# Performance work log

Measured on AMD Instinct MI355X. Metric: run time of the kernel, lower is better.

## Reference

```python
import jax, jax.numpy as jnp
import numpy as np

BATCH = 1048576
D_IN = 4        # d_in=3 spatial dims + 1 time dim
HID = 64
N_HID_STACK = 4  # hidden residual blocks after the first hidden layer
D_OUT = 3
BN_EPS = 1e-5


def _bn(x, gamma, beta):
    # BatchNorm1d in training mode: biased batch statistics over the batch axis
    mu = jnp.mean(x, axis=0)
    var = jnp.var(x, axis=0)
    return gamma * (x - mu) * jax.lax.rsqrt(var + BN_EPS) + beta


def setup_inputs() -> dict:
    key = jax.random.key(0)
    ks = jax.random.split(key, 8)
    s_in = 1.0 / np.sqrt(D_IN)
    s_h = 1.0 / np.sqrt(HID)
    return {
        "x": jax.random.normal(ks[0], (BATCH, D_IN), dtype=jnp.float32),
        "bn0_gamma": jnp.ones((D_IN,), jnp.float32),
        "bn0_beta": jnp.zeros((D_IN,), jnp.float32),
        "W0": jax.random.normal(ks[1], (D_IN, HID), jnp.float32) * s_in,
        "b0": jnp.zeros((HID,), jnp.float32),
        "gamma0": jnp.ones((HID,), jnp.float32),
        "beta0": jnp.zeros((HID,), jnp.float32),
        "W_hid": jax.random.normal(ks[2], (N_HID_STACK, HID, HID), jnp.float32) * s_h,
        "b_hid": jnp.zeros((N_HID_STACK, HID), jnp.float32),
        "gamma_hid": jnp.ones((N_HID_STACK, HID), jnp.float32),
        "beta_hid": jnp.zeros((N_HID_STACK, HID), jnp.float32),
        "Wout": jax.random.normal(ks[3], (HID, D_OUT), jnp.float32) * s_h,
        "bout": jnp.zeros((D_OUT,), jnp.float32),
    }


def reference(x, bn0_gamma, bn0_beta, W0, b0, gamma0, beta0,
              W_hid, b_hid, gamma_hid, beta_hid, Wout, bout):
    # Net.forward (u-network, single patch, batch_normalization=True, tanh):
    #   x = bn0(x)
    #   y = bn(act(Linear0(x)))                 (first hidden layer, no skip)
    #   y = bn_i(act(Linear_i(y))) + y          (residual hidden layers)
    #   y = Linear_out(y)
    h = _bn(x, bn0_gamma, bn0_beta)
    y = _bn(jnp.tanh(h @ W0 + b0), gamma0, beta0)

    def step(y, layer):
        W, b, g, be = layer
        return _bn(jnp.tanh(y @ W + b), g, be) + y, None

    y, _ = jax.lax.scan(step, y, (W_hid, b_hid, gamma_hid, beta_hid))
    return y @ Wout + bout
```

## Files before the change

### kernel.cpp

```cpp
#include <hip/hip_runtime.h>
#include <stdint.h>


#define NROWS 1048576
#define EPS 1e-5f
#define INV_B 9.5367431640625e-07f
#define LOG2E2 2.885390081777927f

typedef __attribute__((ext_vector_type(8))) short bfrag;
typedef __attribute__((ext_vector_type(4))) float facc;
typedef __attribute__((ext_vector_type(4))) float f4v;

__device__ __forceinline__ float bf2f(short s) {
  union { unsigned u; float f; } v;
  v.u = ((unsigned)(unsigned short)s) << 16;
  return v.f;
}
__device__ __forceinline__ short f2bf(float f) {
  union { float f; unsigned u; } v;
  v.f = f;
  unsigned r = v.u + 0x7FFFu + ((v.u >> 16) & 1u);
  return (short)(r >> 16);
}
__device__ __forceinline__ float tanh_fast(float x) {
  float e = __builtin_amdgcn_exp2f(x * LOG2E2);
  return 1.f - 2.f * __builtin_amdgcn_rcpf(e + 1.f);
}

template <int W>
__global__ __launch_bounds__(256) void k_reduce(const float* __restrict__ P,
                                                float* __restrict__ S,
                                                int rows_per_blk) {
  __shared__ float red[256];
  const int tid = threadIdx.x;
  const int col = tid % W;
  const int grp = tid / W;
  const int G = 256 / W;
  size_t r0 = (size_t)blockIdx.x * rows_per_blk;
  float s = 0.f;
  for (int r = grp; r < rows_per_blk; r += G) s += P[(r0 + r) * W + col];
  red[tid] = s;
  __syncthreads();
  if (tid < W) {
    float t = 0.f;
#pragma unroll 4
    for (int g = 0; g < G; ++g) t += red[g * W + tid];
    atomicAdd(&S[tid], t);
  }
}


__global__ __launch_bounds__(256) void k_stats_x(const float* __restrict__ x,
                                                 float* __restrict__ P) {
  __shared__ float red[4][8];
  const int tid = threadIdx.x;
  const int wave = tid >> 6;
  size_t base = (size_t)blockIdx.x * 1024 + tid;
  float s[4] = {0.f, 0.f, 0.f, 0.f}, q[4] = {0.f, 0.f, 0.f, 0.f};
#pragma unroll
  for (int it = 0; it < 4; ++it) {
    f4v v = *(const f4v*)(x + (base + (size_t)it * 256) * 4);
#pragma unroll
    for (int k = 0; k < 4; ++k) { s[k] += v[k]; q[k] = fmaf(v[k], v[k], q[k]); }
  }
#pragma unroll
  for (int off = 32; off > 0; off >>= 1) {
#pragma unroll
    for (int k = 0; k < 4; ++k) {
      s[k] += __shfl_xor(s[k], off);
      q[k] += __shfl_xor(q[k], off);
    }
  }
  if ((tid & 63) == 0) {
#pragma unroll
    for (int k = 0; k < 4; ++k) { red[wave][k] = s[k]; red[wave][4 + k] = q[k]; }
  }
  __syncthreads();
  if (tid < 8)
    P[blockIdx.x * 8 + tid] =
        red[0][tid] + red[1][tid] + red[2][tid] + red[3][tid];
}

__global__ __launch_bounds__(256) void k_stats_z1(
    const float* __restrict__ x, const float* __restrict__ bn0g,
    const float* __restrict__ bn0b, const float* __restrict__ W0,
    const float* __restrict__ b0, const float* __restrict__ sx,
    float* __restrict__ P) {
  __shared__ float red[2][4][64];
  const int tid = threadIdx.x;
  const int lane = tid & 63;
  const int wave = tid >> 6;
  int gw = blockIdx.x * 4 + wave;
  float sc[4], sh[4];
#pragma unroll
  for (int k = 0; k < 4; ++k) {
    float mean = sx[k] * INV_B;
    float var = fmaf(-mean, mean, sx[4 + k] * INV_B);
    float rs = rsqrtf(var + EPS);
    sc[k] = bn0g[k] * rs;
    sh[k] = fmaf(-sc[k], mean, bn0b[k]);
  }
  float w[4];
#pragma unroll
  for (int k = 0; k < 4; ++k) w[k] = W0[k * 64 + lane];
  float bj = b0[lane];
  float s = 0.f, q = 0.f;
  size_t r0 = (size_t)gw * 256;
  for (int r = 0; r < 256; ++r) {
    f4v xv = *(const f4v*)(x + (r0 + r) * 4);
    float acc = bj;
#pragma unroll
    for (int k = 0; k < 4; ++k)
      acc = fmaf(fmaf(xv[k], sc[k], sh[k]), w[k], acc);
    float z = tanh_fast(acc);
    s += z;
    q = fmaf(z, z, q);
  }
  red[0][wave][lane] = s;
  red[1][wave][lane] = q;
  __syncthreads();
  if (tid < 128) {
    int which = tid >> 6, c = tid & 63;
    P[blockIdx.x * 128 + tid] = red[which][0][c] + red[which][1][c] +
                                red[which][2][c] + red[which][3][c];
  }
}

__global__ __launch_bounds__(256) void k_prep(const float* __restrict__ Wh,
                                              short* __restrict__ WT) {
  int idx = blockIdx.x * 256 + threadIdx.x;
  int l = idx >> 12, rem = idx & 4095, k = rem >> 6, c = rem & 63;
  WT[l * 4096 + c * 64 + k] = f2bf(Wh[l * 4096 + k * 64 + c]);
}


__global__ __launch_bounds__(256) void k_first(
    const float* __restrict__ x, const float* __restrict__ bn0g,
    const float* __restrict__ bn0b, const float* __restrict__ W0,
    const float* __restrict__ b0, const float* __restrict__ gamma0,
    const float* __restrict__ beta0, const float* __restrict__ sx,
    const float* __restrict__ s1, const short* __restrict__ WTb,
    const float* __restrict__ bb, float* __restrict__ P,
    short* __restrict__ Y) {
  __shared__ __align__(16) float lds_x[128 * 4];
  __shared__ float lds_W0[256];
  __shared__ float lds_b0[64], lds_A1[64], lds_B1[64], lds_bb[64];
  __shared__ float lds_s0[4], lds_sh0[4];
  __shared__ __align__(16) short lds_y[128 * 72];
  __shared__ float lds_st[128];

  const int tid = threadIdx.x;
  const int lane = tid & 63;
  const int wave = tid >> 6;
  const int l15 = lane & 15;
  const int q = lane >> 4;
  const size_t r0 = (size_t)blockIdx.x * 128;

  if (tid < 128) {
    *(f4v*)(lds_x + tid * 4) = *(const f4v*)(x + (r0 + tid) * 4);
    lds_st[tid] = 0.f;
  }
  lds_W0[tid] = W0[tid];
  if (tid < 64) {
    lds_b0[tid] = b0[tid];
    float mean = s1[tid] * INV_B;
    float var = fmaf(-mean, mean, s1[64 + tid] * INV_B);
    float rs = rsqrtf(var + EPS);
    float A = gamma0[tid] * rs;
    lds_A1[tid] = A;
    lds_B1[tid] = fmaf(-A, mean, beta0[tid]);
    lds_bb[tid] = bb[tid];
  }
  if (tid < 4) {
    float mean = sx[tid] * INV_B;
    float var = fmaf(-mean, mean, sx[4 + tid] * INV_B);
    float rs = rsqrtf(var + EPS);
    float sc = bn0g[tid] * rs;
    lds_s0[tid] = sc;
    lds_sh0[tid] = fmaf(-sc, mean, bn0b[tid]);
  }
  __syncthreads();

  const int wr = wave * 32;
  float sc0[4], sh0[4];
#pragma unroll
  for (int k = 0; k < 4; ++k) { sc0[k] = lds_s0[k]; sh0[k] = lds_sh0[k]; }
  for (int e = 0; e < 32; ++e) {
    int row = wr + e;
    float acc = lds_b0[lane];
#pragma unroll
    for (int k = 0; k < 4; ++k)
      acc = fmaf(fmaf(lds_x[row * 4 + k], sc0[k], sh0[k]),
                 lds_W0[k * 64 + lane], acc);
    float z = tanh_fast(acc);
    lds_y[row * 72 + lane] = f2bf(fmaf(lds_A1[lane], z, lds_B1[lane]));
  }

  bfrag a2[2][2], bw[4][2];
#pragma unroll
  for (int mt = 0; mt < 2; ++mt)
#pragma unroll
    for (int kt = 0; kt < 2; ++kt) {
      a2[mt][kt] =
          *(const bfrag*)&lds_y[(wr + mt * 16 + l15) * 72 + kt * 32 + q * 8];
      *(bfrag*)(Y + (r0 + wr + mt * 16 + l15) * 64 + kt * 32 + q * 8) =
          a2[mt][kt];
    }
#pragma unroll
  for (int nt = 0; nt < 4; ++nt)
#pragma unroll
    for (int kt = 0; kt < 2; ++kt)
      bw[nt][kt] = *(const bfrag*)(WTb + (nt * 16 + l15) * 64 + kt * 32 + q * 8);
  facc acc2[2][4];
#pragma unroll
  for (int mt = 0; mt < 2; ++mt)
#pragma unroll
    for (int nt = 0; nt < 4; ++nt) {
      float bias = lds_bb[nt * 16 + l15];
      acc2[mt][nt][0] = bias; acc2[mt][nt][1] = bias;
      acc2[mt][nt][2] = bias; acc2[mt][nt][3] = bias;
    }
#pragma unroll
  for (int mt = 0; mt < 2; ++mt)
#pragma unroll
    for (int nt = 0; nt < 4; ++nt)
#pragma unroll
      for (int kt = 0; kt < 2; ++kt)
        acc2[mt][nt] = __builtin_amdgcn_mfma_f32_16x16x32_bf16(
            a2[mt][kt], bw[nt][kt], acc2[mt][nt], 0, 0, 0);
#pragma unroll
  for (int nt = 0; nt < 4; ++nt) {
    float s = 0.f, ss = 0.f;
#pragma unroll
    for (int mt = 0; mt < 2; ++mt)
#pragma unroll
      for (int i = 0; i < 4; ++i) {
        float z = tanh_fast(acc2[mt][nt][i]);
        s += z;
        ss = fmaf(z, z, ss);
      }
    s += __shfl_xor(s, 16); s += __shfl_xor(s, 32);
    ss += __shfl_xor(ss, 16); ss += __shfl_xor(ss, 32);
    if (q == 0) {
      atomicAdd(&lds_st[nt * 16 + l15], s);
      atomicAdd(&lds_st[64 + nt * 16 + l15], ss);
    }
  }
  __syncthreads();
  if (tid < 128) P[(size_t)blockIdx.x * 128 + tid] = lds_st[tid];
}

__global__ __launch_bounds__(256) void k_mid(
    short* __restrict__ Y, const short* __restrict__ WTa,
    const float* __restrict__ ba, const float* __restrict__ ga,
    const float* __restrict__ bea, const float* __restrict__ sa,
    const short* __restrict__ WTb, const float* __restrict__ bb,
    float* __restrict__ P) {
  __shared__ __align__(16) short lds_y[128 * 72];
  __shared__ float lds_A[64], lds_Bc[64], lds_ba[64], lds_bb[64];
  __shared__ float lds_st[128];

  const int tid = threadIdx.x;
  const int lane = tid & 63;
  const int wave = tid >> 6;
  const int l15 = lane & 15;
  const int q = lane >> 4;
  const size_t r0 = (size_t)blockIdx.x * 128;

#pragma unroll
  for (int it = 0; it < 4; ++it) {
    int chunk = it * 256 + tid;
    int row = chunk >> 3;
    int c8 = (chunk & 7) * 8;
    *(bfrag*)&lds_y[row * 72 + c8] = *(const bfrag*)(Y + (r0 + row) * 64 + c8);
  }
  if (tid < 128) lds_st[tid] = 0.f;
  if (tid < 64) {
    float mean = sa[tid] * INV_B;
    float var = fmaf(-mean, mean, sa[64 + tid] * INV_B);
    float rs = rsqrtf(var + EPS);
    float A = ga[tid] * rs;
    lds_A[tid] = A;
    lds_Bc[tid] = fmaf(-A, mean, bea[tid]);
    lds_ba[tid] = ba[tid];
    lds_bb[tid] = bb[tid];
  }
  __syncthreads();

  const int wr = wave * 32;
  bfrag a1[2][2], bw[4][2];
#pragma unroll
  for (int mt = 0; mt < 2; ++mt)
#pragma unroll
    for (int kt = 0; kt < 2; ++kt)
      a1[mt][kt] =
          *(const bfrag*)&lds_y[(wr + mt * 16 + l15) * 72 + kt * 32 + q * 8];
#pragma unroll
  for (int nt = 0; nt < 4; ++nt)
#pragma unroll
    for (int kt = 0; kt < 2; ++kt)
      bw[nt][kt] = *(const bfrag*)(WTa + (nt * 16 + l15) * 64 + kt * 32 + q * 8);
  facc acc[2][4];
#pragma unroll
  for (int mt = 0; mt < 2; ++mt)
#pragma unroll
    for (int nt = 0; nt < 4; ++nt) {
      float bias = lds_ba[nt * 16 + l15];
      acc[mt][nt][0] = bias; acc[mt][nt][1] = bias;
      acc[mt][nt][2] = bias; acc[mt][nt][3] = bias;
    }
#pragma unroll
  for (int mt = 0; mt < 2; ++mt)
#pragma unroll
    for (int nt = 0; nt < 4; ++nt)
#pragma unroll
      for (int kt = 0; kt < 2; ++kt)
        acc[mt][nt] = __builtin_amdgcn_mfma_f32_16x16x32_bf16(
            a1[mt][kt], bw[nt][kt], acc[mt][nt], 0, 0, 0);

#pragma unroll
  for (int mt = 0; mt < 2; ++mt)
#pragma unroll
    for (int nt = 0; nt < 4; ++nt) {
      int c = nt * 16 + l15;
      float A = lds_A[c], Bc = lds_Bc[c];
#pragma unroll
      for (int i = 0; i < 4; ++i) {
        int rl = wr + mt * 16 + q * 4 + i;
        float z = tanh_fast(acc[mt][nt][i]);
        float yo = bf2f(lds_y[rl * 72 + c]);
        lds_y[rl * 72 + c] = f2bf(fmaf(A, z, Bc) + yo);
      }
    }

  bfrag a2[2][2];
#pragma unroll
  for (int mt = 0; mt < 2; ++mt)
#pragma unroll
    for (int kt = 0; kt < 2; ++kt) {
      a2[mt][kt] =
          *(const bfrag*)&lds_y[(wr + mt * 16 + l15) * 72 + kt * 32 + q * 8];
      *(bfrag*)(Y + (r0 + wr + mt * 16 + l15) * 64 + kt * 32 + q * 8) =
          a2[mt][kt];
    }
#pragma unroll
  for (int nt = 0; nt < 4; ++nt)
#pragma unroll
    for (int kt = 0; kt < 2; ++kt)
      bw[nt][kt] = *(const bfrag*)(WTb + (nt * 16 + l15) * 64 + kt * 32 + q * 8);
  facc acc2[2][4];
#pragma unroll
  for (int mt = 0; mt < 2; ++mt)
#pragma unroll
    for (int nt = 0; nt < 4; ++nt) {
      float bias = lds_bb[nt * 16 + l15];
      acc2[mt][nt][0] = bias; acc2[mt][nt][1] = bias;
      acc2[mt][nt][2] = bias; acc2[mt][nt][3] = bias;
    }
#pragma unroll
  for (int mt = 0; mt < 2; ++mt)
#pragma unroll
    for (int nt = 0; nt < 4; ++nt)
#pragma unroll
      for (int kt = 0; kt < 2; ++kt)
        acc2[mt][nt] = __builtin_amdgcn_mfma_f32_16x16x32_bf16(
            a2[mt][kt], bw[nt][kt], acc2[mt][nt], 0, 0, 0);
#pragma unroll
  for (int nt = 0; nt < 4; ++nt) {
    float s = 0.f, ss = 0.f;
#pragma unroll
    for (int mt = 0; mt < 2; ++mt)
#pragma unroll
      for (int i = 0; i < 4; ++i) {
        float z = tanh_fast(acc2[mt][nt][i]);
        s += z;
        ss = fmaf(z, z, ss);
      }
    s += __shfl_xor(s, 16); s += __shfl_xor(s, 32);
    ss += __shfl_xor(ss, 16); ss += __shfl_xor(ss, 32);
    if (q == 0) {
      atomicAdd(&lds_st[nt * 16 + l15], s);
      atomicAdd(&lds_st[64 + nt * 16 + l15], ss);
    }
  }
  __syncthreads();
  if (tid < 128) P[(size_t)blockIdx.x * 128 + tid] = lds_st[tid];
}

__global__ __launch_bounds__(256) void k_last(
    const short* __restrict__ Y, const short* __restrict__ WTa,
    const float* __restrict__ ba, const float* __restrict__ ga,
    const float* __restrict__ bea, const float* __restrict__ sa,
    const float* __restrict__ Wout, const float* __restrict__ bout,
    float* __restrict__ out) {
  __shared__ __align__(16) short lds_y[128 * 72];
  __shared__ float lds_A[64], lds_Bc[64], lds_ba[64];
  __shared__ float lds_wo[192];
  __shared__ float lds_bo[3];

  const int tid = threadIdx.x;
  const int lane = tid & 63;
  const int wave = tid >> 6;
  const int l15 = lane & 15;
  const int q = lane >> 4;
  const size_t r0 = (size_t)blockIdx.x * 128;

#pragma unroll
  for (int it = 0; it < 4; ++it) {
    int chunk = it * 256 + tid;
    int row = chunk >> 3;
    int c8 = (chunk & 7) * 8;
    *(bfrag*)&lds_y[row * 72 + c8] = *(const bfrag*)(Y + (r0 + row) * 64 + c8);
  }
  if (tid < 64) {
    float mean = sa[tid] * INV_B;
    float var = fmaf(-mean, mean, sa[64 + tid] * INV_B);
    float rs = rsqrtf(var + EPS);
    float A = ga[tid] * rs;
    lds_A[tid] = A;
    lds_Bc[tid] = fmaf(-A, mean, bea[tid]);
    lds_ba[tid] = ba[tid];
  }
  if (tid < 192) lds_wo[tid] = Wout[tid];
  if (tid < 3) lds_bo[tid] = bout[tid];
  __syncthreads();

  const int wr = wave * 32;
  bfrag a1[2][2], bw[4][2];
#pragma unroll
  for (int mt = 0; mt < 2; ++mt)
#pragma unroll
    for (int kt = 0; kt < 2; ++kt)
      a1[mt][kt] =
          *(const bfrag*)&lds_y[(wr + mt * 16 + l15) * 72 + kt * 32 + q * 8];
#pragma unroll
  for (int nt = 0; nt < 4; ++nt)
#pragma unroll
    for (int kt = 0; kt < 2; ++kt)
      bw[nt][kt] = *(const bfrag*)(WTa + (nt * 16 + l15) * 64 + kt * 32 + q * 8);
  facc acc[2][4];
#pragma unroll
  for (int mt = 0; mt < 2; ++mt)
#pragma unroll
    for (int nt = 0; nt < 4; ++nt) {
      float bias = lds_ba[nt * 16 + l15];
      acc[mt][nt][0] = bias; acc[mt][nt][1] = bias;
      acc[mt][nt][2] = bias; acc[mt][nt][3] = bias;
    }
#pragma unroll
  for (int mt = 0; mt < 2; ++mt)
#pragma unroll
    for (int nt = 0; nt < 4; ++nt)
#pragma unroll
      for (int kt = 0; kt < 2; ++kt)
        acc[mt][nt] = __builtin_amdgcn_mfma_f32_16x16x32_bf16(
            a1[mt][kt], bw[nt][kt], acc[mt][nt], 0, 0, 0);
#pragma unroll
  for (int mt = 0; mt < 2; ++mt)
#pragma unroll
    for (int nt = 0; nt < 4; ++nt) {
      int c = nt * 16 + l15;
      float A = lds_A[c], Bc = lds_Bc[c];
#pragma unroll
      for (int i = 0; i < 4; ++i) {
        int rl = wr + mt * 16 + q * 4 + i;
        float z = tanh_fast(acc[mt][nt][i]);
        float yo = bf2f(lds_y[rl * 72 + c]);
        lds_y[rl * 72 + c] = f2bf(fmaf(A, z, Bc) + yo);
      }
    }
  __syncthreads();

  if (tid < 128) {
    float o0 = lds_bo[0], o1 = lds_bo[1], o2 = lds_bo[2];
#pragma unroll
    for (int jc = 0; jc < 8; ++jc) {
      bfrag v = *(const bfrag*)&lds_y[tid * 72 + jc * 8];
#pragma unroll
      for (int j = 0; j < 8; ++j) {
        float f = bf2f(v[j]);
        int jj = jc * 8 + j;
        o0 = fmaf(f, lds_wo[jj * 3 + 0], o0);
        o1 = fmaf(f, lds_wo[jj * 3 + 1], o1);
        o2 = fmaf(f, lds_wo[jj * 3 + 2], o2);
      }
    }
    size_t ro = (r0 + tid) * 3;
    out[ro] = o0;
    out[ro + 1] = o1;
    out[ro + 2] = o2;
  }
}

extern "C" void kernel_launch(void* const* d_in, const int* in_sizes, int n_in,
                              void* d_out, int out_size, void* d_ws,
                              size_t ws_size, hipStream_t stream) {
  (void)in_sizes; (void)n_in; (void)out_size; (void)ws_size;
  const float* x = (const float*)d_in[0];
  const float* bn0g = (const float*)d_in[1];
  const float* bn0b = (const float*)d_in[2];
  const float* W0 = (const float*)d_in[3];
  const float* b0 = (const float*)d_in[4];
  const float* gamma0 = (const float*)d_in[5];
  const float* beta0 = (const float*)d_in[6];
  const float* Wh = (const float*)d_in[7];
  const float* bh = (const float*)d_in[8];
  const float* gh = (const float*)d_in[9];
  const float* beh = (const float*)d_in[10];
  const float* Wout = (const float*)d_in[11];
  const float* bout = (const float*)d_in[12];
  float* out = (float*)d_out;

  char* ws = (char*)d_ws;
  short* Y = (short*)ws;
  const size_t YB = (size_t)NROWS * 64 * 2;
  float* stats = (float*)(ws + YB);
  float* Sx = stats;
  float* S1 = stats + 8;
  float* S2 = stats + 136;
  float* S3 = stats + 264;
  float* S4 = stats + 392;
  float* S5 = stats + 520;
  short* WT = (short*)(ws + YB + 4096);
  float* P = (float*)(ws + YB + 4096 + 32768);

  hipMemsetAsync(stats, 0, 648 * sizeof(float), stream);
  k_prep<<<64, 256, 0, stream>>>(Wh, WT);
  k_stats_x<<<1024, 256, 0, stream>>>(x, P);
  k_reduce<8><<<8, 256, 0, stream>>>(P, Sx, 128);
  k_stats_z1<<<1024, 256, 0, stream>>>(x, bn0g, bn0b, W0, b0, Sx, P);
  k_reduce<128><<<8, 256, 0, stream>>>(P, S1, 128);
  k_first<<<8192, 256, 0, stream>>>(x, bn0g, bn0b, W0, b0, gamma0, beta0, Sx,
                                    S1, WT, bh, P, Y);
  k_reduce<128><<<64, 256, 0, stream>>>(P, S2, 128);
  k_mid<<<8192, 256, 0, stream>>>(Y, WT, bh, gh, beh, S2, WT + 4096, bh + 64,
                                  P);
  k_reduce<128><<<64, 256, 0, stream>>>(P, S3, 128);
  k_mid<<<8192, 256, 0, stream>>>(Y, WT + 4096, bh + 64, gh + 64, beh + 64, S3,
                                  WT + 2 * 4096, bh + 128, P);
  k_reduce<128><<<64, 256, 0, stream>>>(P, S4, 128);
  k_mid<<<8192, 256, 0, stream>>>(Y, WT + 2 * 4096, bh + 128, gh + 128,
                                  beh + 128, S4, WT + 3 * 4096, bh + 192, P);
  k_reduce<128><<<64, 256, 0, stream>>>(P, S5, 128);
  k_last<<<8192, 256, 0, stream>>>(Y, WT + 3 * 4096, bh + 192, gh + 192,
                                   beh + 192, S5, Wout, bout, out);
}
```

Before: 568.6 us.

## Process four row tiles per block with register prefetch and hoisted weights

Each block of the first, middle and last kernels now handles four 128-row tiles in a loop. Per-column BN coefficients, biases and bf16 weight fragments are loaded into registers once per block instead of through LDS for every tile. The next tile's activations are prefetched into registers while the current tile is computed, and BN statistics accumulate across tiles, so the grid and the partial-sum reductions shrink by four. The output projection is spread over all lanes with a shuffle reduction. Risks are higher register pressure (launch bounds request 3 blocks per SM) and fewer blocks to hide memory latency.

```diff
diff --git a/kernel.cpp b/kernel.cpp
--- a/kernel.cpp
+++ b/kernel.cpp
@@ -6,6 +6,8 @@
 #define EPS 1e-5f
 #define INV_B 9.5367431640625e-07f
 #define LOG2E2 2.885390081777927f
+#define TILES 4
+#define BIGGRID 2048
 
 typedef __attribute__((ext_vector_type(8))) short bfrag;
 typedef __attribute__((ext_vector_type(4))) float facc;
@@ -134,7 +136,7 @@
 }
 
 
-__global__ __launch_bounds__(256) void k_first(
+__global__ __launch_bounds__(256, 3) void k_first(
     const float* __restrict__ x, const float* __restrict__ bn0g,
     const float* __restrict__ bn0b, const float* __restrict__ W0,
     const float* __restrict__ b0, const float* __restrict__ gamma0,
@@ -143,9 +145,6 @@
     const float* __restrict__ bb, float* __restrict__ P,
     short* __restrict__ Y) {
   __shared__ __align__(16) float lds_x[128 * 4];
-  __shared__ float lds_W0[256];
-  __shared__ float lds_b0[64], lds_A1[64], lds_B1[64], lds_bb[64];
-  __shared__ float lds_s0[4], lds_sh0[4];
   __shared__ __align__(16) short lds_y[128 * 72];
   __shared__ float lds_st[128];
 
@@ -154,91 +153,102 @@
   const int wave = tid >> 6;
   const int l15 = lane & 15;
   const int q = lane >> 4;
-  const size_t r0 = (size_t)blockIdx.x * 128;
-
-  if (tid < 128) {
-    *(f4v*)(lds_x + tid * 4) = *(const f4v*)(x + (r0 + tid) * 4);
-    lds_st[tid] = 0.f;
-  }
-  lds_W0[tid] = W0[tid];
-  if (tid < 64) {
-    lds_b0[tid] = b0[tid];
-    float mean = s1[tid] * INV_B;
-    float var = fmaf(-mean, mean, s1[64 + tid] * INV_B);
+  const int wr = wave * 32;
+
+  if (tid < 128) lds_st[tid] = 0.f;
+  float sc0[4], sh0[4];
+#pragma unroll
+  for (int k = 0; k < 4; ++k) {
+    float mean = sx[k] * INV_B;
+    float var = fmaf(-mean, mean, sx[4 + k] * INV_B);
     float rs = rsqrtf(var + EPS);
-    float A = gamma0[tid] * rs;
-    lds_A1[tid] = A;
-    lds_B1[tid] = fmaf(-A, mean, beta0[tid]);
-    lds_bb[tid] = bb[tid];
-  }
-  if (tid < 4) {
-    float mean = sx[tid] * INV_B;
-    float var = fmaf(-mean, mean, sx[4 + tid] * INV_B);
-    float rs = rsqrtf(var + EPS);
-    float sc = bn0g[tid] * rs;
-    lds_s0[tid] = sc;
-    lds_sh0[tid] = fmaf(-sc, mean, bn0b[tid]);
-  }
-  __syncthreads();
-
-  const int wr = wave * 32;
-  float sc0[4], sh0[4];
-#pragma unroll
-  for (int k = 0; k < 4; ++k) { sc0[k] = lds_s0[k]; sh0[k] = lds_sh0[k]; }
-  for (int e = 0; e < 32; ++e) {
-    int row = wr + e;
-    float acc = lds_b0[lane];
-#pragma unroll
-    for (int k = 0; k < 4; ++k)
-      acc = fmaf(fmaf(lds_x[row * 4 + k], sc0[k], sh0[k]),
-                 lds_W0[k * 64 + lane], acc);
-    float z = tanh_fast(acc);
-    lds_y[row * 72 + lane] = f2bf(fmaf(lds_A1[lane], z, lds_B1[lane]));
-  }
-
-  bfrag a2[2][2], bw[4][2];
-#pragma unroll
-  for (int mt = 0; mt < 2; ++mt)
-#pragma unroll
-    for (int kt = 0; kt < 2; ++kt) {
-      a2[mt][kt] =
-          *(const bfrag*)&lds_y[(wr + mt * 16 + l15) * 72 + kt * 32 + q * 8];
-      *(bfrag*)(Y + (r0 + wr + mt * 16 + l15) * 64 + kt * 32 + q * 8) =
-          a2[mt][kt];
-    }
-#pragma unroll
-  for (int nt = 0; nt < 4; ++nt)
+    sc0[k] = bn0g[k] * rs;
+    sh0[k] = fmaf(-sc0[k], mean, bn0b[k]);
+  }
+  float w0c[4];
+#pragma unroll
+  for (int k = 0; k < 4; ++k) w0c[k] = W0[k * 64 + lane];
+  float b0c = b0[lane];
+  float mean1 = s1[lane] * INV_B;
+  float var1 = fmaf(-mean1, mean1, s1[64 + lane] * INV_B);
+  float A1c = gamma0[lane] * rsqrtf(var1 + EPS);
+  float B1c = fmaf(-A1c, mean1, beta0[lane]);
+  float bbv[4];
+  bfrag bwb[4][2];
+#pragma unroll
+  for (int nt = 0; nt < 4; ++nt) {
+    bbv[nt] = bb[nt * 16 + l15];
 #pragma unroll
     for (int kt = 0; kt < 2; ++kt)
-      bw[nt][kt] = *(const bfrag*)(WTb + (nt * 16 + l15) * 64 + kt * 32 + q * 8);
-  facc acc2[2][4];
-#pragma unroll
-  for (int mt = 0; mt < 2; ++mt)
-#pragma unroll
-    for (int nt = 0; nt < 4; ++nt) {
-      float bias = lds_bb[nt * 16 + l15];
-      acc2[mt][nt][0] = bias; acc2[mt][nt][1] = bias;
-      acc2[mt][nt][2] = bias; acc2[mt][nt][3] = bias;
-    }
-#pragma unroll
-  for (int mt = 0; mt < 2; ++mt)
+      bwb[nt][kt] =
+          *(const bfrag*)(WTb + (nt * 16 + l15) * 64 + kt * 32 + q * 8);
+  }
+  __syncthreads();
+
+  float sAcc[4] = {0.f, 0.f, 0.f, 0.f}, qAcc[4] = {0.f, 0.f, 0.f, 0.f};
+  const size_t tbase = (size_t)blockIdx.x * TILES * 128;
+
+  f4v xp;
+  if (lane < 32) xp = *(const f4v*)(x + (tbase + wr + lane) * 4);
+
+#pragma unroll
+  for (int t = 0; t < TILES; ++t) {
+    const size_t r0 = tbase + (size_t)t * 128;
+    if (lane < 32) *(f4v*)&lds_x[(wr + lane) * 4] = xp;
+    if (t + 1 < TILES && lane < 32)
+      xp = *(const f4v*)(x + (r0 + 128 + wr + lane) * 4);
+
+    for (int e = 0; e < 32; ++e) {
+      int row = wr + e;
+      float acc = b0c;
+#pragma unroll
+      for (int k = 0; k < 4; ++k)
+        acc = fmaf(fmaf(lds_x[row * 4 + k], sc0[k], sh0[k]), w0c[k], acc);
+      float z = tanh_fast(acc);
+      lds_y[row * 72 + lane] = f2bf(fmaf(A1c, z, B1c));
+    }
+
+    bfrag af[2][2];
+#pragma unroll
+    for (int mt = 0; mt < 2; ++mt)
+#pragma unroll
+      for (int kt = 0; kt < 2; ++kt) {
+        af[mt][kt] =
+            *(const bfrag*)&lds_y[(wr + mt * 16 + l15) * 72 + kt * 32 + q * 8];
+        *(bfrag*)(Y + (r0 + wr + mt * 16 + l15) * 64 + kt * 32 + q * 8) =
+            af[mt][kt];
+      }
+    facc acc2[2][4];
+#pragma unroll
+    for (int mt = 0; mt < 2; ++mt)
+#pragma unroll
+      for (int nt = 0; nt < 4; ++nt) {
+        acc2[mt][nt][0] = bbv[nt]; acc2[mt][nt][1] = bbv[nt];
+        acc2[mt][nt][2] = bbv[nt]; acc2[mt][nt][3] = bbv[nt];
+      }
+#pragma unroll
+    for (int mt = 0; mt < 2; ++mt)
+#pragma unroll
+      for (int nt = 0; nt < 4; ++nt)
+#pragma unroll
+        for (int kt = 0; kt < 2; ++kt)
+          acc2[mt][nt] = __builtin_amdgcn_mfma_f32_16x16x32_bf16(
+              af[mt][kt], bwb[nt][kt], acc2[mt][nt], 0, 0, 0);
 #pragma unroll
     for (int nt = 0; nt < 4; ++nt)
 #pragma unroll
-      for (int kt = 0; kt < 2; ++kt)
-        acc2[mt][nt] = __builtin_amdgcn_mfma_f32_16x16x32_bf16(
-            a2[mt][kt], bw[nt][kt], acc2[mt][nt], 0, 0, 0);
+      for (int mt = 0; mt < 2; ++mt)
+#pragma unroll
+        for (int i = 0; i < 4; ++i) {
+          float z = tanh_fast(acc2[mt][nt][i]);
+          sAcc[nt] += z;
+          qAcc[nt] = fmaf(z, z, qAcc[nt]);
+        }
+  }
+
 #pragma unroll
   for (int nt = 0; nt < 4; ++nt) {
-    float s = 0.f, ss = 0.f;
-#pragma unroll
-    for (int mt = 0; mt < 2; ++mt)
-#pragma unroll
-      for (int i = 0; i < 4; ++i) {
-        float z = tanh_fast(acc2[mt][nt][i]);
-        s += z;
-        ss = fmaf(z, z, ss);
-      }
+    float s = sAcc[nt], ss = qAcc[nt];
     s += __shfl_xor(s, 16); s += __shfl_xor(s, 32);
     ss += __shfl_xor(ss, 16); ss += __shfl_xor(ss, 32);
     if (q == 0) {
@@ -250,14 +260,13 @@
   if (tid < 128) P[(size_t)blockIdx.x * 128 + tid] = lds_st[tid];
 }
 
-__global__ __launch_bounds__(256) void k_mid(
+__global__ __launch_bounds__(256, 3) void k_mid(
     short* __restrict__ Y, const short* __restrict__ WTa,
     const float* __restrict__ ba, const float* __restrict__ ga,
     const float* __restrict__ bea, const float* __restrict__ sa,
     const short* __restrict__ WTb, const float* __restrict__ bb,
     float* __restrict__ P) {
   __shared__ __align__(16) short lds_y[128 * 72];
-  __shared__ float lds_A[64], lds_Bc[64], lds_ba[64], lds_bb[64];
   __shared__ float lds_st[128];
 
   const int tid = threadIdx.x;
@@ -265,117 +274,137 @@
   const int wave = tid >> 6;
   const int l15 = lane & 15;
   const int q = lane >> 4;
-  const size_t r0 = (size_t)blockIdx.x * 128;
-
-#pragma unroll
-  for (int it = 0; it < 4; ++it) {
-    int chunk = it * 256 + tid;
-    int row = chunk >> 3;
-    int c8 = (chunk & 7) * 8;
-    *(bfrag*)&lds_y[row * 72 + c8] = *(const bfrag*)(Y + (r0 + row) * 64 + c8);
-  }
+  const int wr = wave * 32;
+
   if (tid < 128) lds_st[tid] = 0.f;
-  if (tid < 64) {
-    float mean = sa[tid] * INV_B;
-    float var = fmaf(-mean, mean, sa[64 + tid] * INV_B);
-    float rs = rsqrtf(var + EPS);
-    float A = ga[tid] * rs;
-    lds_A[tid] = A;
-    lds_Bc[tid] = fmaf(-A, mean, bea[tid]);
-    lds_ba[tid] = ba[tid];
-    lds_bb[tid] = bb[tid];
-  }
-  __syncthreads();
-
-  const int wr = wave * 32;
-  bfrag a1[2][2], bw[4][2];
-#pragma unroll
-  for (int mt = 0; mt < 2; ++mt)
-#pragma unroll
-    for (int kt = 0; kt < 2; ++kt)
-      a1[mt][kt] =
-          *(const bfrag*)&lds_y[(wr + mt * 16 + l15) * 72 + kt * 32 + q * 8];
+  float Av[4], Bv[4], bav[4], bbv[4];
+#pragma unroll
+  for (int nt = 0; nt < 4; ++nt) {
+    int c = nt * 16 + l15;
+    float mean = sa[c] * INV_B;
+    float var = fmaf(-mean, mean, sa[64 + c] * INV_B);
+    float A = ga[c] * rsqrtf(var + EPS);
+    Av[nt] = A;
+    Bv[nt] = fmaf(-A, mean, bea[c]);
+    bav[nt] = ba[c];
+    bbv[nt] = bb[c];
+  }
+  bfrag bwa[4][2], bwb[4][2];
 #pragma unroll
   for (int nt = 0; nt < 4; ++nt)
 #pragma unroll
-    for (int kt = 0; kt < 2; ++kt)
-      bw[nt][kt] = *(const bfrag*)(WTa + (nt * 16 + l15) * 64 + kt * 32 + q * 8);
-  facc acc[2][4];
-#pragma unroll
-  for (int mt = 0; mt < 2; ++mt)
-#pragma unroll
-    for (int nt = 0; nt < 4; ++nt) {
-      float bias = lds_ba[nt * 16 + l15];
-      acc[mt][nt][0] = bias; acc[mt][nt][1] = bias;
-      acc[mt][nt][2] = bias; acc[mt][nt][3] = bias;
-    }
-#pragma unroll
-  for (int mt = 0; mt < 2; ++mt)
+    for (int kt = 0; kt < 2; ++kt) {
+      bwa[nt][kt] =
+          *(const bfrag*)(WTa + (nt * 16 + l15) * 64 + kt * 32 + q * 8);
+      bwb[nt][kt] =
+          *(const bfrag*)(WTb + (nt * 16 + l15) * 64 + kt * 32 + q * 8);
+    }
+  __syncthreads();
+
+  float sAcc[4] = {0.f, 0.f, 0.f, 0.f}, qAcc[4] = {0.f, 0.f, 0.f, 0.f};
+  const size_t tbase = (size_t)blockIdx.x * TILES * 128;
+  const int srow = lane >> 3;
+  const int sc8 = (lane & 7) * 8;
+
+  bfrag ld[4];
+  {
+    const size_t g = (tbase + wr + srow) * 64 + sc8;
+#pragma unroll
+    for (int it = 0; it < 4; ++it)
+      ld[it] = *(const bfrag*)(Y + g + (size_t)it * 8 * 64);
+  }
+
+#pragma unroll
+  for (int t = 0; t < TILES; ++t) {
+    const size_t r0 = tbase + (size_t)t * 128;
+#pragma unroll
+    for (int it = 0; it < 4; ++it)
+      *(bfrag*)&lds_y[(wr + it * 8 + srow) * 72 + sc8] = ld[it];
+    if (t + 1 < TILES) {
+      const size_t g = (r0 + 128 + wr + srow) * 64 + sc8;
+#pragma unroll
+      for (int it = 0; it < 4; ++it)
+        ld[it] = *(const bfrag*)(Y + g + (size_t)it * 8 * 64);
+    }
+
+    bfrag af[2][2];
+#pragma unroll
+    for (int mt = 0; mt < 2; ++mt)
+#pragma unroll
+      for (int kt = 0; kt < 2; ++kt)
+        af[mt][kt] =
+            *(const bfrag*)&lds_y[(wr + mt * 16 + l15) * 72 + kt * 32 + q * 8];
+    facc acc[2][4];
+#pragma unroll
+    for (int mt = 0; mt < 2; ++mt)
+#pragma unroll
+      for (int nt = 0; nt < 4; ++nt) {
+        acc[mt][nt][0] = bav[nt]; acc[mt][nt][1] = bav[nt];
+        acc[mt][nt][2] = bav[nt]; acc[mt][nt][3] = bav[nt];
+      }
+#pragma unroll
+    for (int mt = 0; mt < 2; ++mt)
+#pragma unroll
+      for (int nt = 0; nt < 4; ++nt)
+#pragma unroll
+        for (int kt = 0; kt < 2; ++kt)
+          acc[mt][nt] = __builtin_amdgcn_mfma_f32_16x16x32_bf16(
+              af[mt][kt], bwa[nt][kt], acc[mt][nt], 0, 0, 0);
+
+#pragma unroll
+    for (int mt = 0; mt < 2; ++mt)
+#pragma unroll
+      for (int nt = 0; nt < 4; ++nt) {
+        int c = nt * 16 + l15;
+        float A = Av[nt], Bc = Bv[nt];
+#pragma unroll
+        for (int i = 0; i < 4; ++i) {
+          int rl = wr + mt * 16 + q * 4 + i;
+          float z = tanh_fast(acc[mt][nt][i]);
+          float yo = bf2f(lds_y[rl * 72 + c]);
+          lds_y[rl * 72 + c] = f2bf(fmaf(A, z, Bc) + yo);
+        }
+      }
+
+#pragma unroll
+    for (int mt = 0; mt < 2; ++mt)
+#pragma unroll
+      for (int kt = 0; kt < 2; ++kt) {
+        af[mt][kt] =
+            *(const bfrag*)&lds_y[(wr + mt * 16 + l15) * 72 + kt * 32 + q * 8];
+        *(bfrag*)(Y + (r0 + wr + mt * 16 + l15) * 64 + kt * 32 + q * 8) =
+            af[mt][kt];
+      }
+#pragma unroll
+    for (int mt = 0; mt < 2; ++mt)
+#pragma unroll
+      for (int nt = 0; nt < 4; ++nt) {
+        acc[mt][nt][0] = bbv[nt]; acc[mt][nt][1] = bbv[nt];
+        acc[mt][nt][2] = bbv[nt]; acc[mt][nt][3] = bbv[nt];
+      }
+#pragma unroll
+    for (int mt = 0; mt < 2; ++mt)
+#pragma unroll
+      for (int nt = 0; nt < 4; ++nt)
+#pragma unroll
+        for (int kt = 0; kt < 2; ++kt)
+          acc[mt][nt] = __builtin_amdgcn_mfma_f32_16x16x32_bf16(
+              af[mt][kt], bwb[nt][kt], acc[mt][nt], 0, 0, 0);
 #pragma unroll
     for (int nt = 0; nt < 4; ++nt)
 #pragma unroll
-      for (int kt = 0; kt < 2; ++kt)
-        acc[mt][nt] = __builtin_amdgcn_mfma_f32_16x16x32_bf16(
-            a1[mt][kt], bw[nt][kt], acc[mt][nt], 0, 0, 0);
-
-#pragma unroll
-  for (int mt = 0; mt < 2; ++mt)
-#pragma unroll
-    for (int nt = 0; nt < 4; ++nt) {
-      int c = nt * 16 + l15;
-      float A = lds_A[c], Bc = lds_Bc[c];
-#pragma unroll
-      for (int i = 0; i < 4; ++i) {
-        int rl = wr + mt * 16 + q * 4 + i;
-        float z = tanh_fast(acc[mt][nt][i]);
-        float yo = bf2f(lds_y[rl * 72 + c]);
-        lds_y[rl * 72 + c] = f2bf(fmaf(A, z, Bc) + yo);
-      }
-    }
-
-  bfrag a2[2][2];
-#pragma unroll
-  for (int mt = 0; mt < 2; ++mt)
-#pragma unroll
-    for (int kt = 0; kt < 2; ++kt) {
-      a2[mt][kt] =
-          *(const bfrag*)&lds_y[(wr + mt * 16 + l15) * 72 + kt * 32 + q * 8];
-      *(bfrag*)(Y + (r0 + wr + mt * 16 + l15) * 64 + kt * 32 + q * 8) =
-          a2[mt][kt];
-    }
-#pragma unroll
-  for (int nt = 0; nt < 4; ++nt)
-#pragma unroll
-    for (int kt = 0; kt < 2; ++kt)
-      bw[nt][kt] = *(const bfrag*)(WTb + (nt * 16 + l15) * 64 + kt * 32 + q * 8);
-  facc acc2[2][4];
-#pragma unroll
-  for (int mt = 0; mt < 2; ++mt)
-#pragma unroll
-    for (int nt = 0; nt < 4; ++nt) {
-      float bias = lds_bb[nt * 16 + l15];
-      acc2[mt][nt][0] = bias; acc2[mt][nt][1] = bias;
-      acc2[mt][nt][2] = bias; acc2[mt][nt][3] = bias;
-    }
-#pragma unroll
-  for (int mt = 0; mt < 2; ++mt)
-#pragma unroll
-    for (int nt = 0; nt < 4; ++nt)
-#pragma unroll
-      for (int kt = 0; kt < 2; ++kt)
-        acc2[mt][nt] = __builtin_amdgcn_mfma_f32_16x16x32_bf16(
-            a2[mt][kt], bw[nt][kt], acc2[mt][nt], 0, 0, 0);
+      for (int mt = 0; mt < 2; ++mt)
+#pragma unroll
+        for (int i = 0; i < 4; ++i) {
+          float z = tanh_fast(acc[mt][nt][i]);
+          sAcc[nt] += z;
+          qAcc[nt] = fmaf(z, z, qAcc[nt]);
+        }
+  }
+
 #pragma unroll
   for (int nt = 0; nt < 4; ++nt) {
-    float s = 0.f, ss = 0.f;
-#pragma unroll
-    for (int mt = 0; mt < 2; ++mt)
-#pragma unroll
-      for (int i = 0; i < 4; ++i) {
-        float z = tanh_fast(acc2[mt][nt][i]);
-        s += z;
-        ss = fmaf(z, z, ss);
-      }
+    float s = sAcc[nt], ss = qAcc[nt];
     s += __shfl_xor(s, 16); s += __shfl_xor(s, 32);
     ss += __shfl_xor(ss, 16); ss += __shfl_xor(ss, 32);
     if (q == 0) {
@@ -387,108 +416,133 @@
   if (tid < 128) P[(size_t)blockIdx.x * 128 + tid] = lds_st[tid];
 }
 
-__global__ __launch_bounds__(256) void k_last(
+__global__ __launch_bounds__(256, 3) void k_last(
     const short* __restrict__ Y, const short* __restrict__ WTa,
     const float* __restrict__ ba, const float* __restrict__ ga,
     const float* __restrict__ bea, const float* __restrict__ sa,
     const float* __restrict__ Wout, const float* __restrict__ bout,
     float* __restrict__ out) {
   __shared__ __align__(16) short lds_y[128 * 72];
-  __shared__ float lds_A[64], lds_Bc[64], lds_ba[64];
   __shared__ float lds_wo[192];
-  __shared__ float lds_bo[3];
 
   const int tid = threadIdx.x;
   const int lane = tid & 63;
   const int wave = tid >> 6;
   const int l15 = lane & 15;
   const int q = lane >> 4;
-  const size_t r0 = (size_t)blockIdx.x * 128;
-
-#pragma unroll
-  for (int it = 0; it < 4; ++it) {
-    int chunk = it * 256 + tid;
-    int row = chunk >> 3;
-    int c8 = (chunk & 7) * 8;
-    *(bfrag*)&lds_y[row * 72 + c8] = *(const bfrag*)(Y + (r0 + row) * 64 + c8);
-  }
-  if (tid < 64) {
-    float mean = sa[tid] * INV_B;
-    float var = fmaf(-mean, mean, sa[64 + tid] * INV_B);
-    float rs = rsqrtf(var + EPS);
-    float A = ga[tid] * rs;
-    lds_A[tid] = A;
-    lds_Bc[tid] = fmaf(-A, mean, bea[tid]);
-    lds_ba[tid] = ba[tid];
-  }
+  const int wr = wave * 32;
+
   if (tid < 192) lds_wo[tid] = Wout[tid];
-  if (tid < 3) lds_bo[tid] = bout[tid];
-  __syncthreads();
-
-  const int wr = wave * 32;
-  bfrag a1[2][2], bw[4][2];
-#pragma unroll
-  for (int mt = 0; mt < 2; ++mt)
+  float Av[4], Bv[4], bav[4];
+#pragma unroll
+  for (int nt = 0; nt < 4; ++nt) {
+    int c = nt * 16 + l15;
+    float mean = sa[c] * INV_B;
+    float var = fmaf(-mean, mean, sa[64 + c] * INV_B);
+    float A = ga[c] * rsqrtf(var + EPS);
+    Av[nt] = A;
+    Bv[nt] = fmaf(-A, mean, bea[c]);
+    bav[nt] = ba[c];
+  }
+  bfrag bwa[4][2];
+#pragma unroll
+  for (int nt = 0; nt < 4; ++nt)
 #pragma unroll
     for (int kt = 0; kt < 2; ++kt)
-      a1[mt][kt] =
-          *(const bfrag*)&lds_y[(wr + mt * 16 + l15) * 72 + kt * 32 + q * 8];
-#pragma unroll
-  for (int nt = 0; nt < 4; ++nt)
-#pragma unroll
-    for (int kt = 0; kt < 2; ++kt)
-      bw[nt][kt] = *(const bfrag*)(WTa + (nt * 16 + l15) * 64 + kt * 32 + q * 8);
-  facc acc[2][4];
-#pragma unroll
-  for (int mt = 0; mt < 2; ++mt)
-#pragma unroll
-    for (int nt = 0; nt < 4; ++nt) {
-      float bias = lds_ba[nt * 16 + l15];
-      acc[mt][nt][0] = bias; acc[mt][nt][1] = bias;
-      acc[mt][nt][2] = bias; acc[mt][nt][3] = bias;
-    }
-#pragma unroll
-  for (int mt = 0; mt < 2; ++mt)
-#pragma unroll
-    for (int nt = 0; nt < 4; ++nt)
+      bwa[nt][kt] =
+          *(const bfrag*)(WTa + (nt * 16 + l15) * 64 + kt * 32 + q * 8);
+  float bo0 = bout[0], bo1 = bout[1], bo2 = bout[2];
+  __syncthreads();
+
+  const size_t tbase = (size_t)blockIdx.x * TILES * 128;
+  const int srow = lane >> 3;
+  const int sc8 = (lane & 7) * 8;
+
+  bfrag ld[4];
+  {
+    const size_t g = (tbase + wr + srow) * 64 + sc8;
+#pragma unroll
+    for (int it = 0; it < 4; ++it)
+      ld[it] = *(const bfrag*)(Y + g + (size_t)it * 8 * 64);
+  }
+
+#pragma unroll
+  for (int t = 0; t < TILES; ++t) {
+    const size_t r0 = tbase + (size_t)t * 128;
+#pragma unroll
+    for (int it = 0; it < 4; ++it)
+      *(bfrag*)&lds_y[(wr + it * 8 + srow) * 72 + sc8] = ld[it];
+    if (t + 1 < TILES) {
+      const size_t g = (r0 + 128 + wr + srow) * 64 + sc8;
+#pragma unroll
+      for (int it = 0; it < 4; ++it)
+        ld[it] = *(const bfrag*)(Y + g + (size_t)it * 8 * 64);
+    }
+
+    bfrag af[2][2];
+#pragma unroll
+    for (int mt = 0; mt < 2; ++mt)
 #pragma unroll
       for (int kt = 0; kt < 2; ++kt)
-        acc[mt][nt] = __builtin_amdgcn_mfma_f32_16x16x32_bf16(
-            a1[mt][kt], bw[nt][kt], acc[mt][nt], 0, 0, 0);
-#pragma unroll
-  for (int mt = 0; mt < 2; ++mt)
-#pragma unroll
-    for (int nt = 0; nt < 4; ++nt) {
-      int c = nt * 16 + l15;
-      float A = lds_A[c], Bc = lds_Bc[c];
-#pragma unroll
-      for (int i = 0; i < 4; ++i) {
-        int rl = wr + mt * 16 + q * 4 + i;
-        float z = tanh_fast(acc[mt][nt][i]);
-        float yo = bf2f(lds_y[rl * 72 + c]);
-        lds_y[rl * 72 + c] = f2bf(fmaf(A, z, Bc) + yo);
-      }
-    }
-  __syncthreads();
-
-  if (tid < 128) {
-    float o0 = lds_bo[0], o1 = lds_bo[1], o2 = lds_bo[2];
-#pragma unroll
-    for (int jc = 0; jc < 8; ++jc) {
-      bfrag v = *(const bfrag*)&lds_y[tid * 72 + jc * 8];
-#pragma unroll
-      for (int j = 0; j < 8; ++j) {
-        float f = bf2f(v[j]);
-        int jj = jc * 8 + j;
-        o0 = fmaf(f, lds_wo[jj * 3 + 0], o0);
-        o1 = fmaf(f, lds_wo[jj * 3 + 1], o1);
-        o2 = fmaf(f, lds_wo[jj * 3 + 2], o2);
-      }
-    }
-    size_t ro = (r0 + tid) * 3;
-    out[ro] = o0;
-    out[ro + 1] = o1;
-    out[ro + 2] = o2;
+        af[mt][kt] =
+            *(const bfrag*)&lds_y[(wr + mt * 16 + l15) * 72 + kt * 32 + q * 8];
+    facc acc[2][4];
+#pragma unroll
+    for (int mt = 0; mt < 2; ++mt)
+#pragma unroll
+      for (int nt = 0; nt < 4; ++nt) {
+        acc[mt][nt][0] = bav[nt]; acc[mt][nt][1] = bav[nt];
+        acc[mt][nt][2] = bav[nt]; acc[mt][nt][3] = bav[nt];
+      }
+#pragma unroll
+    for (int mt = 0; mt < 2; ++mt)
+#pragma unroll
+      for (int nt = 0; nt < 4; ++nt)
+#pragma unroll
+        for (int kt = 0; kt < 2; ++kt)
+          acc[mt][nt] = __builtin_amdgcn_mfma_f32_16x16x32_bf16(
+              af[mt][kt], bwa[nt][kt], acc[mt][nt], 0, 0, 0);
+#pragma unroll
+    for (int mt = 0; mt < 2; ++mt)
+#pragma unroll
+      for (int nt = 0; nt < 4; ++nt) {
+        int c = nt * 16 + l15;
+        float A = Av[nt], Bc = Bv[nt];
+#pragma unroll
+        for (int i = 0; i < 4; ++i) {
+          int rl = wr + mt * 16 + q * 4 + i;
+          float z = tanh_fast(acc[mt][nt][i]);
+          float yo = bf2f(lds_y[rl * 72 + c]);
+          lds_y[rl * 72 + c] = f2bf(fmaf(A, z, Bc) + yo);
+        }
+      }
+
+    {
+      int row = wr + (lane >> 1);
+      int cb = (lane & 1) * 32;
+      float o0 = 0.f, o1 = 0.f, o2 = 0.f;
+#pragma unroll
+      for (int jc = 0; jc < 4; ++jc) {
+        bfrag v = *(const bfrag*)&lds_y[row * 72 + cb + jc * 8];
+#pragma unroll
+        for (int j = 0; j < 8; ++j) {
+          float f = bf2f(v[j]);
+          int jj = cb + jc * 8 + j;
+          o0 = fmaf(f, lds_wo[jj * 3 + 0], o0);
+          o1 = fmaf(f, lds_wo[jj * 3 + 1], o1);
+          o2 = fmaf(f, lds_wo[jj * 3 + 2], o2);
+        }
+      }
+      o0 += __shfl_xor(o0, 1);
+      o1 += __shfl_xor(o1, 1);
+      o2 += __shfl_xor(o2, 1);
+      if ((lane & 1) == 0) {
+        size_t ro = (r0 + row) * 3;
+        out[ro] = o0 + bo0;
+        out[ro + 1] = o1 + bo1;
+        out[ro + 2] = o2 + bo2;
+      }
+    }
   }
 }
 
@@ -530,18 +584,18 @@
   k_reduce<8><<<8, 256, 0, stream>>>(P, Sx, 128);
   k_stats_z1<<<1024, 256, 0, stream>>>(x, bn0g, bn0b, W0, b0, Sx, P);
   k_reduce<128><<<8, 256, 0, stream>>>(P, S1, 128);
-  k_first<<<8192, 256, 0, stream>>>(x, bn0g, bn0b, W0, b0, gamma0, beta0, Sx,
-                                    S1, WT, bh, P, Y);
-  k_reduce<128><<<64, 256, 0, stream>>>(P, S2, 128);
-  k_mid<<<8192, 256, 0, stream>>>(Y, WT, bh, gh, beh, S2, WT + 4096, bh + 64,
-                                  P);
-  k_reduce<128><<<64, 256, 0, stream>>>(P, S3, 128);
-  k_mid<<<8192, 256, 0, stream>>>(Y, WT + 4096, bh + 64, gh + 64, beh + 64, S3,
-                                  WT + 2 * 4096, bh + 128, P);
-  k_reduce<128><<<64, 256, 0, stream>>>(P, S4, 128);
-  k_mid<<<8192, 256, 0, stream>>>(Y, WT + 2 * 4096, bh + 128, gh + 128,
-                                  beh + 128, S4, WT + 3 * 4096, bh + 192, P);
-  k_reduce<128><<<64, 256, 0, stream>>>(P, S5, 128);
-  k_last<<<8192, 256, 0, stream>>>(Y, WT + 3 * 4096, bh + 192, gh + 192,
-                                   beh + 192, S5, Wout, bout, out);
-}
+  k_first<<<BIGGRID, 256, 0, stream>>>(x, bn0g, bn0b, W0, b0, gamma0, beta0,
+                                       Sx, S1, WT, bh, P, Y);
+  k_reduce<128><<<16, 256, 0, stream>>>(P, S2, 128);
+  k_mid<<<BIGGRID, 256, 0, stream>>>(Y, WT, bh, gh, beh, S2, WT + 4096,
+                                     bh + 64, P);
+  k_reduce<128><<<16, 256, 0, stream>>>(P, S3, 128);
+  k_mid<<<BIGGRID, 256, 0, stream>>>(Y, WT + 4096, bh + 64, gh + 64, beh + 64,
+                                     S3, WT + 2 * 4096, bh + 128, P);
+  k_reduce<128><<<16, 256, 0, stream>>>(P, S4, 128);
+  k_mid<<<BIGGRID, 256, 0, stream>>>(Y, WT + 2 * 4096, bh + 128, gh + 128,
+                                     beh + 128, S4, WT + 3 * 4096, bh + 192, P);
+  k_reduce<128><<<16, 256, 0, stream>>>(P, S5, 128);
+  k_last<<<BIGGRID, 256, 0, stream>>>(Y, WT + 3 * 4096, bh + 192, gh + 192,
+                                      beh + 192, S5, Wout, bout, out);
+}
```

Result: slower. 600.1 us (+5.6%).
